# Optimization experiments

Hardware: AMD Instinct MI355X
Metric: run time of the kernel (lower is better)

Reference implementation:

```python
import jax, jax.numpy as jnp
import numpy as np

G, N, F, H, B, L = 4, 1024, 256, 256, 32, 4


def setup_inputs() -> dict:
    key = jax.random.key(0)
    ks = jax.random.split(key, 8)
    batch_xs = jax.random.normal(ks[0], (G, N, F), dtype=jnp.float32)
    # dense (preprocessed/normalized) adjacency; scale ~1/N keeps activations stable
    batch_as = jax.random.uniform(ks[1], (G, N, N), dtype=jnp.float32) / N
    w_in = jax.random.normal(ks[2], (F, H), dtype=jnp.float32) * 0.05
    b_in = jnp.zeros((H,), dtype=jnp.float32)
    gcn_w = jax.random.normal(ks[3], (L, H, H), dtype=jnp.float32) * 0.05
    gcn_b = jnp.zeros((L, H), dtype=jnp.float32)
    graph_idx = jax.random.randint(ks[4], (B,), 0, G)
    cp_mask = jax.random.randint(ks[5], (B, N), 0, 2).astype(bool)
    return {"batch_xs": batch_xs, "batch_as": batch_as, "w_in": w_in, "b_in": b_in,
            "gcn_w": gcn_w, "gcn_b": gcn_b, "graph_idx": graph_idx, "cp_mask": cp_mask}


def reference(batch_xs, batch_as, w_in, b_in, gcn_w, gcn_b, graph_idx, cp_mask):
    # gather_nd: select per-example graph features and adjacency
    X = batch_xs[graph_idx]          # [B, N, F]
    A = batch_as[graph_idx]          # [B, N, N]
    # GNN input dense layer (relu); dropout is identity at inference
    x = jax.nn.relu(X @ w_in + b_in)  # [B, N, H]
    res = x                           # residual from post-input activations
    # GCNConv stack: act(A @ x @ W + b); relu for all but final tanh layer
    for i in range(L - 1):
        x = jax.nn.relu(jnp.einsum('bnm,bmh->bnh', A, x) @ gcn_w[i] + gcn_b[i])
    x = jnp.tanh(jnp.einsum('bnm,bmh->bnh', A, x) @ gcn_w[L - 1] + gcn_b[L - 1])
    x = x + res
    # ragged boolean_mask + reduce_mean over nodes == masked mean
    m = cp_mask.astype(x.dtype)       # [B, N]
    denom = jnp.maximum(jnp.sum(m, axis=1, keepdims=True), 1.0)
    return jnp.sum(x * m[..., None], axis=1) / denom  # [B, H]
```

## Files before the change

### kernel.cpp

```cpp
#include <hip/hip_runtime.h>
#include <math.h>

#define G 4
#define NN 1024
#define FF 256
#define HH 256
#define BB 32
#define LL 4

typedef __attribute__((ext_vector_type(8))) short short8;
typedef __attribute__((ext_vector_type(8))) unsigned short ushort8;
typedef __attribute__((ext_vector_type(4))) unsigned short ushort4v;
typedef __attribute__((ext_vector_type(4))) float floatx4;

__device__ inline unsigned short f2bf(float f) {
  union { float f; unsigned u; } x; x.f = f;
  unsigned r = x.u + 0x7fffu + ((x.u >> 16) & 1u);
  return (unsigned short)(r >> 16);
}
__device__ inline float bf2f(unsigned short u) {
  union { unsigned u; float f; } x; x.u = (unsigned)u << 16;
  return x.f;
}

__device__ void in_tile(int job, const float* __restrict__ X,
                        const float* __restrict__ w_in,
                        const float* __restrict__ b_in,
                        unsigned short* __restrict__ xbf,
                        unsigned short* __restrict__ h0bf, unsigned short* As,
                        unsigned short* Bs, int t) {
  const int nt_ = job & 3, mt = (job >> 2) & 15, g = job >> 6;
  const int m0 = mt * 64, n0 = nt_ * 64;
  const int lane = t & 63, w = t >> 6;
  const int wm = w & 1, wn = w >> 1;
  const int l16 = lane & 15, quad = lane >> 4;

  floatx4 acc[2][2];
#pragma unroll
  for (int i = 0; i < 2; ++i)
#pragma unroll
    for (int j = 0; j < 2; ++j) acc[i][j] = (floatx4){0.f, 0.f, 0.f, 0.f};

  for (int tt = 0; tt < 4; ++tt) {
    const int kb = tt * 64;
    __syncthreads();
#pragma unroll
    for (int i = 0; i < 2; ++i) {
      const int q = t + i * 256;
      const int row = q >> 3, c8 = q & 7;
      const float* Af =
          X + (long)g * NN * FF + (long)(m0 + row) * FF + kb + c8 * 8;
      float4 f0 = *(const float4*)Af;
      float4 f1 = *(const float4*)(Af + 4);
      ushort8 v;
      v[0] = f2bf(f0.x); v[1] = f2bf(f0.y); v[2] = f2bf(f0.z); v[3] = f2bf(f0.w);
      v[4] = f2bf(f1.x); v[5] = f2bf(f1.y); v[6] = f2bf(f1.z); v[7] = f2bf(f1.w);
      *(ushort8*)&As[row * 72 + c8 * 8] = v;
    }
    {
      const int row = t >> 2;
      const int c0 = (t & 3) * 16;
#pragma unroll
      for (int j = 0; j < 4; ++j) {
        float4 f = *(const float4*)&w_in[(long)(kb + row) * HH + n0 + c0 + j * 4];
        Bs[(c0 + j * 4 + 0) * 72 + row] = f2bf(f.x);
        Bs[(c0 + j * 4 + 1) * 72 + row] = f2bf(f.y);
        Bs[(c0 + j * 4 + 2) * 72 + row] = f2bf(f.z);
        Bs[(c0 + j * 4 + 3) * 72 + row] = f2bf(f.w);
      }
    }
    __syncthreads();
#pragma unroll
    for (int kk = 0; kk < 64; kk += 32) {
      const int ko = kk + quad * 8;
      short8 a0 = *(const short8*)&As[(wm * 32 + l16) * 72 + ko];
      short8 a1 = *(const short8*)&As[(wm * 32 + 16 + l16) * 72 + ko];
      short8 b0 = *(const short8*)&Bs[(wn * 32 + l16) * 72 + ko];
      short8 b1 = *(const short8*)&Bs[(wn * 32 + 16 + l16) * 72 + ko];
      acc[0][0] = __builtin_amdgcn_mfma_f32_16x16x32_bf16(a0, b0, acc[0][0], 0, 0, 0);
      acc[0][1] = __builtin_amdgcn_mfma_f32_16x16x32_bf16(a0, b1, acc[0][1], 0, 0, 0);
      acc[1][0] = __builtin_amdgcn_mfma_f32_16x16x32_bf16(a1, b0, acc[1][0], 0, 0, 0);
      acc[1][1] = __builtin_amdgcn_mfma_f32_16x16x32_bf16(a1, b1, acc[1][1], 0, 0, 0);
    }
  }

#pragma unroll
  for (int i = 0; i < 2; ++i) {
#pragma unroll
    for (int j = 0; j < 2; ++j) {
      const int n = n0 + wn * 32 + j * 16 + l16;
      const int mB = m0 + wm * 32 + i * 16 + quad * 4;
      const float bv = b_in[n];
#pragma unroll
      for (int r = 0; r < 4; ++r) {
        const unsigned short pv = f2bf(fmaxf(acc[i][j][r] + bv, 0.f));
        xbf[(long)g * NN * HH + (long)(mB + r) * HH + n] = pv;
        h0bf[(long)g * NN * HH + (long)(mB + r) * HH + n] = pv;
      }
    }
  }
}

__device__ void mask_job(int b, const void* __restrict__ cp_mask,
                         float* __restrict__ fmask, float* __restrict__ denom,
                         int t) {
  const unsigned char* bytes = (const unsigned char*)cp_mask;
  __shared__ int fmt;
  __shared__ float red[256];
  if (t == 0) {
    int any = 0;
    for (int i = 0; i < 256; ++i)
      if ((i & 3) && bytes[i]) any = 1;
    fmt = any ? 0 : 1;
  }
  __syncthreads();
  float cnt = 0.f;
  for (int n = t; n < NN; n += 256) {
    float v;
    if (fmt)
      v = ((const int*)cp_mask)[b * NN + n] ? 1.f : 0.f;
    else
      v = bytes[b * NN + n] ? 1.f : 0.f;
    fmask[b * NN + n] = v;
    cnt += v;
  }
  red[t] = cnt;
  __syncthreads();
  for (int s = 128; s > 0; s >>= 1) {
    if (t < s) red[t] += red[t + s];
    __syncthreads();
  }
  if (t == 0) denom[b] = fmaxf(red[0], 1.f);
}

__device__ void gw_job(int j, const float* __restrict__ gcn_w,
                       unsigned short* __restrict__ gwT, int t) {
  const int l = j >> 4, r0 = (j & 15) * 16;
  const float* src = gcn_w + (long)l * HH * HH;
  unsigned short* dst = gwT + (long)l * HH * HH;
  unsigned short vv[16];
#pragma unroll
  for (int rr = 0; rr < 16; ++rr) vv[rr] = f2bf(src[(long)(r0 + rr) * HH + t]);
  *(ushort8*)&dst[(long)t * HH + r0] = *(ushort8*)&vv[0];
  *(ushort8*)&dst[(long)t * HH + r0 + 8] = *(ushort8*)&vv[8];
}

__global__ __launch_bounds__(256) void pre_kernel(
    const float* __restrict__ batch_as, unsigned short* __restrict__ Abf,
    const float* __restrict__ batch_xs, const float* __restrict__ w_in,
    const float* __restrict__ b_in, unsigned short* __restrict__ xbf,
    unsigned short* __restrict__ h0bf, const float* __restrict__ gcn_w,
    unsigned short* __restrict__ gwT, const void* __restrict__ cp_mask,
    float* __restrict__ fmask, float* __restrict__ denom,
    float* __restrict__ out) {
  __shared__ __align__(16) unsigned short As[64 * 72];
  __shared__ __align__(16) unsigned short Bs[64 * 72];
  const int b = blockIdx.x, t = threadIdx.x;
  if (b < 1024) {
    const long idx = ((long)b * 256 + t) * 16;
#pragma unroll
    for (int h = 0; h < 2; ++h) {
      float4 f0 = *(const float4*)&batch_as[idx + h * 8];
      float4 f1 = *(const float4*)&batch_as[idx + h * 8 + 4];
      ushort8 v;
      v[0] = f2bf(f0.x); v[1] = f2bf(f0.y); v[2] = f2bf(f0.z); v[3] = f2bf(f0.w);
      v[4] = f2bf(f1.x); v[5] = f2bf(f1.y); v[6] = f2bf(f1.z); v[7] = f2bf(f1.w);
      *(ushort8*)&Abf[idx + h * 8] = v;
    }
  } else if (b < 1280) {
    in_tile(b - 1024, batch_xs, w_in, b_in, xbf, h0bf, As, Bs, t);
  } else if (b < 1344) {
    gw_job(b - 1280, gcn_w, gwT, t);
  } else if (b < 1376) {
    mask_job(b - 1344, cp_mask, fmask, denom, t);
  } else {
    for (int i = 0; i < 32; ++i) out[i * 256 + t] = 0.f;
  }
}

__global__ __launch_bounds__(256) void g1_kernel(
    const unsigned short* __restrict__ xbf,
    const unsigned short* __restrict__ WT,
    unsigned short* __restrict__ yT) {
  __shared__ __align__(16) unsigned short As[64 * 72];
  __shared__ __align__(16) unsigned short Bs[64 * 72];
  const int n0 = blockIdx.x * 64;
  const int m0 = blockIdx.y * 64;
  const int g = blockIdx.z;
  const int t = threadIdx.x;
  const int lane = t & 63, w = t >> 6;
  const int wm = w & 1, wn = w >> 1;
  const int l16 = lane & 15, quad = lane >> 4;

  const unsigned short* Ab = xbf + (long)g * NN * HH;

  ushort8 pa[2], pb[2];
  auto load_tile = [&](int tt) {
    const int kb = tt * 64;
#pragma unroll
    for (int i = 0; i < 2; ++i) {
      const int q = t + i * 256;
      const int row = q >> 3, c8 = q & 7;
      pa[i] = *(const ushort8*)&Ab[(long)(m0 + row) * HH + kb + c8 * 8];
      pb[i] = *(const ushort8*)&WT[(long)(n0 + row) * HH + kb + c8 * 8];
    }
  };
  auto store_tile = [&]() {
#pragma unroll
    for (int i = 0; i < 2; ++i) {
      const int q = t + i * 256;
      const int row = q >> 3, c8 = q & 7;
      *(ushort8*)&As[row * 72 + c8 * 8] = pa[i];
      *(ushort8*)&Bs[row * 72 + c8 * 8] = pb[i];
    }
  };

  floatx4 acc[2][2];
#pragma unroll
  for (int i = 0; i < 2; ++i)
#pragma unroll
    for (int j = 0; j < 2; ++j) acc[i][j] = (floatx4){0.f, 0.f, 0.f, 0.f};

  load_tile(0);
  for (int tt = 0; tt < 4; ++tt) {
    __syncthreads();
    store_tile();
    __syncthreads();
    if (tt + 1 < 4) load_tile(tt + 1);
#pragma unroll
    for (int kk = 0; kk < 64; kk += 32) {
      const int ko = kk + quad * 8;
      short8 a0 = *(const short8*)&As[(wm * 32 + l16) * 72 + ko];
      short8 a1 = *(const short8*)&As[(wm * 32 + 16 + l16) * 72 + ko];
      short8 b0 = *(const short8*)&Bs[(wn * 32 + l16) * 72 + ko];
      short8 b1 = *(const short8*)&Bs[(wn * 32 + 16 + l16) * 72 + ko];
      acc[0][0] = __builtin_amdgcn_mfma_f32_16x16x32_bf16(a0, b0, acc[0][0], 0, 0, 0);
      acc[0][1] = __builtin_amdgcn_mfma_f32_16x16x32_bf16(a0, b1, acc[0][1], 0, 0, 0);
      acc[1][0] = __builtin_amdgcn_mfma_f32_16x16x32_bf16(a1, b0, acc[1][0], 0, 0, 0);
      acc[1][1] = __builtin_amdgcn_mfma_f32_16x16x32_bf16(a1, b1, acc[1][1], 0, 0, 0);
    }
  }

#pragma unroll
  for (int i = 0; i < 2; ++i) {
#pragma unroll
    for (int j = 0; j < 2; ++j) {
      const int n = n0 + wn * 32 + j * 16 + l16;
      const int mB = m0 + wm * 32 + i * 16 + quad * 4;
      ushort4v pv;
#pragma unroll
      for (int r = 0; r < 4; ++r) pv[r] = f2bf(acc[i][j][r]);
      *(ushort4v*)&yT[(long)g * HH * NN + (long)n * NN + mB] = pv;
    }
  }
}

template <int ACT>
__global__ __launch_bounds__(256) void g2_kernel(
    const unsigned short* __restrict__ Abf,
    const unsigned short* __restrict__ yT, const float* __restrict__ bias,
    const unsigned short* __restrict__ h0bf,
    unsigned short* __restrict__ outbf) {
  __shared__ __align__(16) unsigned short As[32 * 72];
  __shared__ __align__(16) unsigned short Bs[64 * 72];
  const int n0 = blockIdx.x * 64;
  const int m0 = blockIdx.y * 32;
  const int g = blockIdx.z;
  const int t = threadIdx.x;
  const int lane = t & 63, w = t >> 6;
  const int wm = w & 1, wn = w >> 1;
  const int l16 = lane & 15, quad = lane >> 4;

  const unsigned short* Ag = Abf + (long)g * NN * NN + (long)m0 * NN;
  const unsigned short* Bg = yT + (long)g * HH * NN + (long)n0 * NN;

  ushort8 pa, pb[2];
  auto load_tile = [&](int tt) {
    const int kb = tt * 64;
    {
      const int row = t >> 3, c8 = t & 7;
      pa = *(const ushort8*)&Ag[(long)row * NN + kb + c8 * 8];
    }
#pragma unroll
    for (int i = 0; i < 2; ++i) {
      const int q = t + i * 256;
      const int row = q >> 3, c8 = q & 7;
      pb[i] = *(const ushort8*)&Bg[(long)row * NN + kb + c8 * 8];
    }
  };
  auto store_tile = [&]() {
    {
      const int row = t >> 3, c8 = t & 7;
      *(ushort8*)&As[row * 72 + c8 * 8] = pa;
    }
#pragma unroll
    for (int i = 0; i < 2; ++i) {
      const int q = t + i * 256;
      const int row = q >> 3, c8 = q & 7;
      *(ushort8*)&Bs[row * 72 + c8 * 8] = pb[i];
    }
  };

  floatx4 acc[2];
  acc[0] = (floatx4){0.f, 0.f, 0.f, 0.f};
  acc[1] = (floatx4){0.f, 0.f, 0.f, 0.f};

  load_tile(0);
  for (int tt = 0; tt < 16; ++tt) {
    __syncthreads();
    store_tile();
    __syncthreads();
    if (tt + 1 < 16) load_tile(tt + 1);
#pragma unroll
    for (int kk = 0; kk < 64; kk += 32) {
      const int ko = kk + quad * 8;
      short8 a = *(const short8*)&As[(wm * 16 + l16) * 72 + ko];
      short8 b0 = *(const short8*)&Bs[(wn * 32 + l16) * 72 + ko];
      short8 b1 = *(const short8*)&Bs[(wn * 32 + 16 + l16) * 72 + ko];
      acc[0] = __builtin_amdgcn_mfma_f32_16x16x32_bf16(a, b0, acc[0], 0, 0, 0);
      acc[1] = __builtin_amdgcn_mfma_f32_16x16x32_bf16(a, b1, acc[1], 0, 0, 0);
    }
  }

#pragma unroll
  for (int j = 0; j < 2; ++j) {
    const int n = n0 + wn * 32 + j * 16 + l16;
    const int mB = m0 + wm * 16 + quad * 4;
    const float bv = bias[n];
#pragma unroll
    for (int r = 0; r < 4; ++r) {
      const long idx = (long)g * NN * HH + (long)(mB + r) * HH + n;
      if (ACT == 1) {
        outbf[idx] = f2bf(fmaxf(acc[j][r] + bv, 0.f));
      } else {
        outbf[idx] = f2bf(tanhf(acc[j][r] + bv) + bf2f(h0bf[idx]));
      }
    }
  }
}

__global__ __launch_bounds__(256) void mean_kernel(
    const unsigned short* __restrict__ zbf, const float* __restrict__ fmask,
    const float* __restrict__ denom, const int* __restrict__ gidx,
    float* __restrict__ out) {
  const int job = blockIdx.x;
  const int t = threadIdx.x;
  const int b = job >> 3, ch = job & 7;
  const int g = gidx[b];
  const unsigned short* z = zbf + (long)g * NN * HH;
  const int n0 = ch * 128;
  float s = 0.f;
  for (int n = n0; n < n0 + 128; ++n) {
    float m = fmask[b * NN + n];
    if (m != 0.f) s += bf2f(z[(long)n * HH + t]);
  }
  atomicAdd(&out[b * HH + t], s / denom[b]);
}

extern "C" void kernel_launch(void* const* d_in, const int* in_sizes, int n_in,
                              void* d_out, int out_size, void* d_ws,
                              size_t ws_size, hipStream_t stream) {
  (void)in_sizes; (void)n_in; (void)out_size; (void)ws_size;
  const float* batch_xs = (const float*)d_in[0];
  const float* batch_as = (const float*)d_in[1];
  const float* w_in = (const float*)d_in[2];
  const float* b_in = (const float*)d_in[3];
  const float* gcn_w = (const float*)d_in[4];
  const float* gcn_b = (const float*)d_in[5];
  const int* graph_idx = (const int*)d_in[6];
  const void* cp_mask = d_in[7];
  float* out = (float*)d_out;

  char* p = (char*)d_ws;
  unsigned short* Abf = (unsigned short*)p;  p += (long)G * NN * NN * 2;
  unsigned short* gwT = (unsigned short*)p;  p += (long)LL * HH * HH * 2;
  unsigned short* xbf = (unsigned short*)p;  p += (long)G * NN * HH * 2;
  unsigned short* h0bf = (unsigned short*)p; p += (long)G * NN * HH * 2;
  unsigned short* yT = (unsigned short*)p;   p += (long)G * HH * NN * 2;
  unsigned short* zbf = (unsigned short*)p;  p += (long)G * NN * HH * 2;
  float* fmask = (float*)p;                  p += (long)BB * NN * 4;
  float* denom = (float*)p;                  p += BB * 4;

  pre_kernel<<<1377, 256, 0, stream>>>(batch_as, Abf, batch_xs, w_in, b_in,
                                       xbf, h0bf, gcn_w, gwT, cp_mask, fmask,
                                       denom, out);

  for (int l = 0; l < LL; ++l) {
    g1_kernel<<<dim3(4, 16, G), 256, 0, stream>>>(
        xbf, gwT + (long)l * HH * HH, yT);
    if (l < LL - 1)
      g2_kernel<1><<<dim3(4, 32, G), 256, 0, stream>>>(
          Abf, yT, gcn_b + (long)l * HH, nullptr, xbf);
    else
      g2_kernel<0><<<dim3(4, 32, G), 256, 0, stream>>>(
          Abf, yT, gcn_b + (long)l * HH, h0bf, zbf);
  }

  mean_kernel<<<BB * 8, 256, 0, stream>>>(zbf, fmask, denom, graph_idx, out);
}
```

Measured before the change: 168.5 us.

## Fuse masked mean into final GCN layer and widen g2 K-tile to 128

The masked-mean reduction is folded into the epilogue of the last aggregation kernel. Each block reduces its tile's masked contributions with lane shuffles and atomically adds them into the output for every batch entry that maps to its graph. This removes the separate mean kernel and the bf16 round-trip of the final activations. The g2 K-tile is also doubled from 64 to 128, which halves the loop iterations and barriers at the cost of more shared memory and registers per block. The fused epilogue loops over all 32 batch entries per block and issues many more atomics.

```diff
diff --git a/kernel.cpp b/kernel.cpp
--- a/kernel.cpp
+++ b/kernel.cpp
@@ -259,10 +259,11 @@
 __global__ __launch_bounds__(256) void g2_kernel(
     const unsigned short* __restrict__ Abf,
     const unsigned short* __restrict__ yT, const float* __restrict__ bias,
-    const unsigned short* __restrict__ h0bf,
-    unsigned short* __restrict__ outbf) {
-  __shared__ __align__(16) unsigned short As[32 * 72];
-  __shared__ __align__(16) unsigned short Bs[64 * 72];
+    const unsigned short* __restrict__ h0bf, unsigned short* __restrict__ xbf,
+    const float* __restrict__ fmask, const float* __restrict__ denom,
+    const int* __restrict__ gidx, float* __restrict__ out) {
+  __shared__ __align__(16) unsigned short As[32 * 136];
+  __shared__ __align__(16) unsigned short Bs[64 * 136];
   const int n0 = blockIdx.x * 64;
   const int m0 = blockIdx.y * 32;
   const int g = blockIdx.z;
@@ -274,30 +275,34 @@
   const unsigned short* Ag = Abf + (long)g * NN * NN + (long)m0 * NN;
   const unsigned short* Bg = yT + (long)g * HH * NN + (long)n0 * NN;
 
-  ushort8 pa, pb[2];
+  ushort8 pa[2], pb[4];
   auto load_tile = [&](int tt) {
-    const int kb = tt * 64;
-    {
-      const int row = t >> 3, c8 = t & 7;
-      pa = *(const ushort8*)&Ag[(long)row * NN + kb + c8 * 8];
-    }
+    const int kb = tt * 128;
 #pragma unroll
     for (int i = 0; i < 2; ++i) {
       const int q = t + i * 256;
-      const int row = q >> 3, c8 = q & 7;
+      const int row = q >> 4, c8 = q & 15;
+      pa[i] = *(const ushort8*)&Ag[(long)row * NN + kb + c8 * 8];
+    }
+#pragma unroll
+    for (int i = 0; i < 4; ++i) {
+      const int q = t + i * 256;
+      const int row = q >> 4, c8 = q & 15;
       pb[i] = *(const ushort8*)&Bg[(long)row * NN + kb + c8 * 8];
     }
   };
   auto store_tile = [&]() {
-    {
-      const int row = t >> 3, c8 = t & 7;
-      *(ushort8*)&As[row * 72 + c8 * 8] = pa;
-    }
 #pragma unroll
     for (int i = 0; i < 2; ++i) {
       const int q = t + i * 256;
-      const int row = q >> 3, c8 = q & 7;
-      *(ushort8*)&Bs[row * 72 + c8 * 8] = pb[i];
+      const int row = q >> 4, c8 = q & 15;
+      *(ushort8*)&As[row * 136 + c8 * 8] = pa[i];
+    }
+#pragma unroll
+    for (int i = 0; i < 4; ++i) {
+      const int q = t + i * 256;
+      const int row = q >> 4, c8 = q & 15;
+      *(ushort8*)&Bs[row * 136 + c8 * 8] = pb[i];
     }
   };
 
@@ -306,55 +311,65 @@
   acc[1] = (floatx4){0.f, 0.f, 0.f, 0.f};
 
   load_tile(0);
-  for (int tt = 0; tt < 16; ++tt) {
+  for (int tt = 0; tt < 8; ++tt) {
     __syncthreads();
     store_tile();
     __syncthreads();
-    if (tt + 1 < 16) load_tile(tt + 1);
-#pragma unroll
-    for (int kk = 0; kk < 64; kk += 32) {
+    if (tt + 1 < 8) load_tile(tt + 1);
+#pragma unroll
+    for (int kk = 0; kk < 128; kk += 32) {
       const int ko = kk + quad * 8;
-      short8 a = *(const short8*)&As[(wm * 16 + l16) * 72 + ko];
-      short8 b0 = *(const short8*)&Bs[(wn * 32 + l16) * 72 + ko];
-      short8 b1 = *(const short8*)&Bs[(wn * 32 + 16 + l16) * 72 + ko];
+      short8 a = *(const short8*)&As[(wm * 16 + l16) * 136 + ko];
+      short8 b0 = *(const short8*)&Bs[(wn * 32 + l16) * 136 + ko];
+      short8 b1 = *(const short8*)&Bs[(wn * 32 + 16 + l16) * 136 + ko];
       acc[0] = __builtin_amdgcn_mfma_f32_16x16x32_bf16(a, b0, acc[0], 0, 0, 0);
       acc[1] = __builtin_amdgcn_mfma_f32_16x16x32_bf16(a, b1, acc[1], 0, 0, 0);
     }
   }
 
-#pragma unroll
-  for (int j = 0; j < 2; ++j) {
-    const int n = n0 + wn * 32 + j * 16 + l16;
-    const int mB = m0 + wm * 16 + quad * 4;
-    const float bv = bias[n];
-#pragma unroll
-    for (int r = 0; r < 4; ++r) {
-      const long idx = (long)g * NN * HH + (long)(mB + r) * HH + n;
-      if (ACT == 1) {
-        outbf[idx] = f2bf(fmaxf(acc[j][r] + bv, 0.f));
-      } else {
-        outbf[idx] = f2bf(tanhf(acc[j][r] + bv) + bf2f(h0bf[idx]));
+  if (ACT == 1) {
+#pragma unroll
+    for (int j = 0; j < 2; ++j) {
+      const int n = n0 + wn * 32 + j * 16 + l16;
+      const int mB = m0 + wm * 16 + quad * 4;
+      const float bv = bias[n];
+#pragma unroll
+      for (int r = 0; r < 4; ++r)
+        xbf[(long)g * NN * HH + (long)(mB + r) * HH + n] =
+            f2bf(fmaxf(acc[j][r] + bv, 0.f));
+    }
+  } else {
+    const int mB0 = m0 + wm * 16 + quad * 4;
+    float zv[2][4];
+#pragma unroll
+    for (int j = 0; j < 2; ++j) {
+      const int n = n0 + wn * 32 + j * 16 + l16;
+      const float bv = bias[n];
+#pragma unroll
+      for (int r = 0; r < 4; ++r) {
+        const long idx = (long)g * NN * HH + (long)(mB0 + r) * HH + n;
+        zv[j][r] = tanhf(acc[j][r] + bv) + bf2f(h0bf[idx]);
       }
     }
-  }
-}
-
-__global__ __launch_bounds__(256) void mean_kernel(
-    const unsigned short* __restrict__ zbf, const float* __restrict__ fmask,
-    const float* __restrict__ denom, const int* __restrict__ gidx,
-    float* __restrict__ out) {
-  const int job = blockIdx.x;
-  const int t = threadIdx.x;
-  const int b = job >> 3, ch = job & 7;
-  const int g = gidx[b];
-  const unsigned short* z = zbf + (long)g * NN * HH;
-  const int n0 = ch * 128;
-  float s = 0.f;
-  for (int n = n0; n < n0 + 128; ++n) {
-    float m = fmask[b * NN + n];
-    if (m != 0.f) s += bf2f(z[(long)n * HH + t]);
-  }
-  atomicAdd(&out[b * HH + t], s / denom[b]);
+    for (int b = 0; b < BB; ++b) {
+      if (gidx[b] != g) continue;
+      const float invd = 1.f / denom[b];
+      float m4[4];
+#pragma unroll
+      for (int r = 0; r < 4; ++r) m4[r] = fmask[b * NN + mB0 + r];
+#pragma unroll
+      for (int j = 0; j < 2; ++j) {
+        float p = m4[0] * zv[j][0] + m4[1] * zv[j][1] + m4[2] * zv[j][2] +
+                  m4[3] * zv[j][3];
+        p += __shfl_xor(p, 16);
+        p += __shfl_xor(p, 32);
+        if (quad == 0) {
+          const int n = n0 + wn * 32 + j * 16 + l16;
+          atomicAdd(&out[b * HH + n], p * invd);
+        }
+      }
+    }
+  }
 }
 
 extern "C" void kernel_launch(void* const* d_in, const int* in_sizes, int n_in,
@@ -377,7 +392,6 @@
   unsigned short* xbf = (unsigned short*)p;  p += (long)G * NN * HH * 2;
   unsigned short* h0bf = (unsigned short*)p; p += (long)G * NN * HH * 2;
   unsigned short* yT = (unsigned short*)p;   p += (long)G * HH * NN * 2;
-  unsigned short* zbf = (unsigned short*)p;  p += (long)G * NN * HH * 2;
   float* fmask = (float*)p;                  p += (long)BB * NN * 4;
   float* denom = (float*)p;                  p += BB * 4;
 
@@ -390,11 +404,11 @@
         xbf, gwT + (long)l * HH * HH, yT);
     if (l < LL - 1)
       g2_kernel<1><<<dim3(4, 32, G), 256, 0, stream>>>(
-          Abf, yT, gcn_b + (long)l * HH, nullptr, xbf);
+          Abf, yT, gcn_b + (long)l * HH, nullptr, xbf, nullptr, nullptr,
+          nullptr, nullptr);
     else
       g2_kernel<0><<<dim3(4, 32, G), 256, 0, stream>>>(
-          Abf, yT, gcn_b + (long)l * HH, h0bf, zbf);
-  }
-
-  mean_kernel<<<BB * 8, 256, 0, stream>>>(zbf, fmask, denom, graph_idx, out);
-}
+          Abf, yT, gcn_b + (long)l * HH, h0bf, nullptr, fmask, denom,
+          graph_idx, out);
+  }
+}
```

Result: faster. 149.8 us (median of 2 runs) (-11.1%).
